# Kernel optimization log

Hardware: AMD Instinct MI355X
Metric: run time of the kernel (lower is better)

## Reference

```python
import jax, jax.numpy as jnp
import numpy as np
from jax import lax

EPS_RADIUS = 1e-3  # eps_radius from __init__


def setup_inputs() -> dict:
    key = jax.random.key(0)
    ks = jax.random.split(key, 8)
    Bsz, L, H, N, O = 16, 4096, 512, 512, 512
    n_pairs = N // 2
    return {
        "input": jax.random.normal(ks[0], (Bsz, L, H), dtype=jnp.float32),
        "state": jnp.zeros((Bsz, N), dtype=jnp.float32),
        "S": 0.1 * jax.random.normal(ks[1], (N, N), dtype=jnp.float32),
        "rho_raw": 0.01 * jax.random.normal(ks[2], (n_pairs,), dtype=jnp.float32),
        "theta": 0.01 * jax.random.normal(ks[3], (n_pairs,), dtype=jnp.float32),
        "K12_raw": 0.5 * jax.random.normal(ks[4], (N, H), dtype=jnp.float32),
        "K21_raw": 0.5 * jax.random.normal(ks[5], (O, N), dtype=jnp.float32),
        "K22_raw": 0.5 * jax.random.normal(ks[6], (O, H), dtype=jnp.float32),
        "log_gamma": jnp.zeros((), dtype=jnp.float32),  # gamma = 1.0
    }


def _dense_ssm_matrices(S, rho_raw, theta, K12_raw, K21_raw, K22_raw, log_gamma):
    N = S.shape[0]
    n_pairs = N // 2
    # K11 structured: block-diag 2x2 rotation-scaling blocks
    rho = jax.nn.sigmoid(rho_raw) * (1.0 - EPS_RADIUS)
    c, s = jnp.cos(theta), jnp.sin(theta)
    ii = jnp.arange(n_pairs) * 2
    K11 = jnp.zeros((N, N), dtype=S.dtype)
    K11 = (K11.at[ii, ii].set(rho * c)
               .at[ii, ii + 1].set(-rho * s)
               .at[ii + 1, ii].set(rho * s)
               .at[ii + 1, ii + 1].set(rho * c))
    # assemble full K and spectrally normalize (exact norm via SVD)
    K_raw = jnp.block([[K11, K12_raw], [K21_raw, K22_raw]])
    sigma = jnp.maximum(jnp.linalg.norm(K_raw, ord=2), 1e-5)
    K = K_raw / (sigma + 0.002)
    K11n = K[:N, :N]
    K12n = K[:N, N:]
    K21n = K[N:, :N]
    K22n = K[N:, N:]
    gamma = jnp.exp(log_gamma)
    Sinv = jnp.linalg.inv(S)
    A = Sinv @ K11n @ S          # (N, N)
    B = gamma * (Sinv @ K12n)    # (N, H)
    C = K21n @ S                 # (O, N)
    D = gamma * K22n             # (O, H)
    return A, B, C, D


def reference(input, state, S, rho_raw, theta, K12_raw, K21_raw, K22_raw, log_gamma):
    A, B, C, D = _dense_ssm_matrices(S, rho_raw, theta, K12_raw, K21_raw, K22_raw, log_gamma)
    u = input  # (Bsz, L, H)
    Bu = jnp.einsum('blh,nh->lbn', u, B)  # precompute input projections, (L, Bsz, N)

    def step(x, bu_t):
        x_new = x @ A.T + bu_t  # (Bsz, N)
        return x_new, x_new

    _, xs = lax.scan(step, state, Bu)  # xs: (L, Bsz, N), states x_1..x_L
    # y_t = C x_t + D u_t uses pre-states x_0..x_{L-1}
    pre = jnp.concatenate([state[None], xs[:-1]], axis=0)  # (L, Bsz, N)
    y = jnp.einsum('lbn,on->blo', pre, C) + jnp.einsum('blh,oh->blo', u, D)
    return y
```

## Files before the change

kernel.cpp:

```cpp
#include <hip/hip_runtime.h>
#include <stdint.h>


#define LM 40
#define CHUNK 128
#define WARM 12
#define LBLK 32

typedef float f32x4 __attribute__((ext_vector_type(4)));
typedef __bf16 bf16x8 __attribute__((ext_vector_type(8)));
typedef unsigned int u32;
typedef unsigned long long u64;
typedef unsigned short u16;

static __device__ __forceinline__ u16 f2bf(float f){
  u32 u = __float_as_uint(f);
  u32 r = (u + 0x7fffu + ((u >> 16) & 1u)) >> 16;
  return (u16)r;
}

static __device__ __forceinline__ float kraw_at(int i, int j,
    const float* rho_raw, const float* theta,
    const float* K12, const float* K21, const float* K22){
  if (i < 512){
    if (j < 512){
      if ((i >> 1) != (j >> 1)) return 0.f;
      int p = i >> 1;
      float rho = (1.f / (1.f + expf(-rho_raw[p]))) * 0.999f;
      float c = cosf(theta[p]), s = sinf(theta[p]);
      return ((i & 1) == 0) ? (((j & 1) == 0) ? rho * c : -rho * s)
                            : (((j & 1) == 0) ? rho * s :  rho * c);
    }
    return K12[i * 512 + (j - 512)];
  }
  if (j < 512) return K21[(i - 512) * 512 + j];
  return K22[(i - 512) * 512 + (j - 512)];
}

__global__ __launch_bounds__(256) void build_KT(const float* rho_raw, const float* theta,
    const float* K12, const float* K21, const float* K22, u16* KTbf,
    double* alpha, double* nrm2, u64* rec){
  if (blockIdx.x == 4096){
    int t = threadIdx.x;
    if (t < 64){ alpha[t] = 0.0; nrm2[t] = 0.0; }
    for (int i = t; i < 2048; i += 256) rec[i] = 0ull;
    return;
  }
  int idx = blockIdx.x * 256 + threadIdx.x;
  int j = idx >> 10, i = idx & 1023;
  KTbf[idx] = f2bf(kraw_at(i, j, rho_raw, theta, K12, K21, K22));
}

__global__ __launch_bounds__(256, 1) void lanczos_G(const float* __restrict__ G,
    u64* rec, double* alphaOut, double* nrm2Out){
  __shared__ __align__(16) float vl[1024];
  __shared__ float red[8];
  int t = threadIdx.x, wave = t >> 6, lane = t & 63;
  int row0 = blockIdx.x * 32;

  f32x4 greg[8][4];
  {
    const float* gbase = G + (size_t)(row0 + wave * 8) * 1024 + lane * 4;
    #pragma unroll
    for (int rr = 0; rr < 8; ++rr)
      #pragma unroll
      for (int i2 = 0; i2 < 4; ++i2)
        greg[rr][i2] = *(const f32x4*)(gbase + (size_t)rr * 1024 + i2 * 256);
  }

  float vprevreg[4] = {0.f, 0.f, 0.f, 0.f};
  float n2tot;
  {
    float s = 0.f;
    #pragma unroll
    for (int k = 0; k < 4; ++k){
      int i = t + 256 * k;
      float v = sinf(0.613f * (float)i + 0.271f) + 0.3f * sinf(0.0247f * (float)i + 1.3f);
      vl[i] = v;
      s += v * v;
    }
    #pragma unroll
    for (int off = 32; off; off >>= 1) s += __shfl_down(s, off);
    if (lane == 0) red[wave] = s;
    __syncthreads();
    n2tot = (red[0] + red[1]) + (red[2] + red[3]);
  }
  float scal = 1.f / sqrtf(n2tot);
  float betacoef = 0.f;

  for (int j = 1; j <= LM; ++j){
    u64* rb = rec + ((j & 1) ? 0 : 1024);
    {
      f32x4 vreg[4];
      #pragma unroll
      for (int i2 = 0; i2 < 4; ++i2)
        vreg[i2] = *((const f32x4*)vl + lane + 64 * i2);
      u64 myrec = 0ull;
      #pragma unroll
      for (int rr = 0; rr < 8; ++rr){
        float s = 0.f;
        #pragma unroll
        for (int i2 = 0; i2 < 4; ++i2){
          f32x4 g = greg[rr][i2], v = vreg[i2];
          s += g[0] * v[0] + g[1] * v[1] + g[2] * v[2] + g[3] * v[3];
        }
        #pragma unroll
        for (int off = 32; off; off >>= 1) s += __shfl_xor(s, off);
        if (lane == rr)
          myrec = ((u64)(u32)j << 32) | (u64)__float_as_uint(s);
      }
      if (lane < 8)
        __hip_atomic_store(&rb[row0 + wave * 8 + lane], myrec,
                           __ATOMIC_RELAXED, __HIP_MEMORY_SCOPE_AGENT);
    }

    float yr[4], vr[4];
    {
      u32 need = 0xFu;
      u64 rv[4];
      while (need){
        #pragma unroll
        for (int k = 0; k < 4; ++k){
          if (need & (1u << k)){
            u64 r = __hip_atomic_load(&rb[t + 256 * k],
                                      __ATOMIC_RELAXED, __HIP_MEMORY_SCOPE_AGENT);
            if ((u32)(r >> 32) == (u32)j){ rv[k] = r; need &= ~(1u << k); }
          }
        }
        if (need) __builtin_amdgcn_s_sleep(1);
      }
      #pragma unroll
      for (int k = 0; k < 4; ++k){
        yr[k] = __uint_as_float((u32)rv[k]);
        vr[k] = vl[t + 256 * k];
      }
    }

    float dotp = 0.f;
    #pragma unroll
    for (int k = 0; k < 4; ++k) dotp += vr[k] * yr[k];
    #pragma unroll
    for (int off = 32; off; off >>= 1) dotp += __shfl_down(dotp, off);
    if (lane == 0) red[wave] = dotp;
    __syncthreads();
    float dot = (red[0] + red[1]) + (red[2] + red[3]);
    float alpha_f = dot * scal * scal;

    float n2 = 0.f;
    #pragma unroll
    for (int k = 0; k < 4; ++k){
      float vh = vr[k] * scal;
      float wv = yr[k] * scal - alpha_f * vh - betacoef * vprevreg[k];
      vprevreg[k] = vh;
      vl[t + 256 * k] = wv;
      n2 += wv * wv;
    }
    #pragma unroll
    for (int off = 32; off; off >>= 1) n2 += __shfl_down(n2, off);
    if (lane == 0) red[4 + wave] = n2;
    __syncthreads();
    n2tot = (red[4] + red[5]) + (red[6] + red[7]);
    if (n2tot < 1e-30f) n2tot = 1e-30f;

    if (blockIdx.x == 0 && t == 0){
      alphaOut[j] = (double)alpha_f;
      nrm2Out[j]  = (double)n2tot;
    }
    betacoef = sqrtf(n2tot);
    scal = 1.f / betacoef;
  }
}

__global__ __launch_bounds__(256) void finalize_sigma(const double* alpha, const double* beta2,
    const float* rho_raw, const float* theta, const float* log_gamma,
    float* scal, float2* coef){
  __shared__ double sa[LM], sb2[LM + 1];
  __shared__ float sh_inv;
  int t = threadIdx.x;
  if (t < LM) sa[t] = alpha[t];
  if (t < LM + 1) sb2[t] = beta2[t];
  __syncthreads();
  if (t < 64){
    int lane = t;
    double lo = sa[0], hi = sa[0], bmax = 0.0;
    for (int i = 0; i < LM; ++i){
      if (sa[i] > lo) lo = sa[i];
      double bl = (i > 0) ? sqrt(fmax(sb2[i], 0.0)) : 0.0;
      double br = (i < LM - 1) ? sqrt(fmax(sb2[i + 1], 0.0)) : 0.0;
      double g = sa[i] + bl + br;
      if (g > hi) hi = g;
      if (i < LM - 1 && sb2[i + 1] > bmax) bmax = sb2[i + 1];
    }
    hi = hi + 1e-6 * fabs(hi) + 1e-20;
    lo = lo - 1e-6 * fabs(lo) - 1e-20;
    double pivmin = 1e-30 * bmax + 1e-300;
    for (int round = 0; round < 6; ++round){
      double x = lo + (hi - lo) * ((double)(lane + 1) / 65.0);
      double d = sa[0] - x; int cnt = (d < 0.0);
      for (int i = 1; i < LM; ++i){
        if (fabs(d) < pivmin) d = -pivmin;
        d = (sa[i] - x) - sb2[i] / d;
        cnt += (d < 0.0);
      }
      unsigned long long mk = __ballot(cnt >= LM);
      int bpos = (mk == 0ULL) ? 64 : (__ffsll((unsigned long long)mk) - 1);
      double xlo = __shfl(x, (bpos == 0) ? 0 : bpos - 1);
      double xhi = __shfl(x, (bpos == 64) ? 63 : bpos);
      double nlo = (bpos == 0) ? lo : xlo;
      double nhi = (bpos == 64) ? hi : xhi;
      lo = nlo; hi = nhi;
    }
    if (lane == 0){
      double lam = 0.5 * (lo + hi);
      double sig = (lam > 0.0) ? sqrt(lam) : 0.0;
      if (sig < 1e-5) sig = 1e-5;
      double spp = sig + 0.002;
      float inv = (float)(1.0 / spp);
      float g = expf(log_gamma[0]);
      scal[0] = inv; scal[1] = g; scal[2] = g * inv;
      sh_inv = inv;
    }
  }
  __syncthreads();
  float inv = sh_inv;
  float rho = (1.f / (1.f + expf(-rho_raw[t]))) * 0.999f;
  float c = cosf(theta[t]), s = sinf(theta[t]);
  coef[t] = make_float2(rho * c * inv, rho * s * inv);
}

__global__ __launch_bounds__(256) void prep_main(const float4* u4, u16* X,
    const float4* k12_4, u16* W12, const float* S, const float* state, float* w0){
  int blk = blockIdx.x;
  if (blk < 32768){
    long g = (long)blk * 256 + threadIdx.x;
    float4 v = u4[g];
    int h4 = (int)(g & 127);
    long row = g >> 7;
    u16* dst = X + row * 1024 + 512 + h4 * 4;
    u32 lo = (u32)f2bf(v.x) | ((u32)f2bf(v.y) << 16);
    u32 hi = (u32)f2bf(v.z) | ((u32)f2bf(v.w) << 16);
    *((uint2*)dst) = make_uint2(lo, hi);
  } else if (blk < 32768 + 256){
    long g = (long)(blk - 32768) * 256 + threadIdx.x;
    float4 v = k12_4[g];
    u32 lo = (u32)f2bf(v.x) | ((u32)f2bf(v.y) << 16);
    u32 hi = (u32)f2bf(v.z) | ((u32)f2bf(v.w) << 16);
    ((uint2*)W12)[g] = make_uint2(lo, hi);
  } else {
    int idx = (blk - 33024) * 256 + threadIdx.x;
    int b = idx >> 9, n = idx & 511;
    const float* sr = S + n * 512;
    const float* st = state + b * 512;
    float acc = 0.f;
    for (int m2 = 0; m2 < 512; ++m2) acc += sr[m2] * st[m2];
    w0[idx] = acc;
  }
}

__global__ __launch_bounds__(256) void build_wcat(const float* K21, const float* K22,
    const float* scal, u16* W){
  int idx = blockIdx.x * 256 + threadIdx.x;
  int o = idx >> 10, c = idx & 1023;
  float inv = scal[0], gi = scal[2];
  float v = (c < 512) ? K21[o * 512 + c] * inv : K22[o * 512 + (c - 512)] * gi;
  W[idx] = f2bf(v);
}

__global__ __launch_bounds__(256) void scan_kernel(const u32* Bu, const float2* coef,
    const float* w0, const float* scal, u16* X){
  int b = blockIdx.x >> 5;
  int c = blockIdx.x & 31;
  int p = threadIdx.x;
  float2 ab = coef[p];
  float gi = scal[2];
  int t0 = c * CHUNK;
  float wx, wy; int t;
  if (c == 0){ wx = w0[b * 512 + 2 * p]; wy = w0[b * 512 + 2 * p + 1]; t = 0; }
  else { wx = 0.f; wy = 0.f; t = t0 - WARM; }
  const u32* bub = Bu + (size_t)b * 4096 * 256;
  u16* xb = X + (size_t)b * 4096 * 1024;
  for (; t < t0; ++t){
    u32 v = bub[(size_t)t * 256 + p];
    float bx = __uint_as_float(v << 16);
    float by = __uint_as_float(v & 0xffff0000u);
    float nx = ab.x * wx - ab.y * wy + gi * bx;
    float ny = ab.y * wx + ab.x * wy + gi * by;
    wx = nx; wy = ny;
  }
  for (; t < t0 + CHUNK; ++t){
    u32 pk = (u32)f2bf(wx) | ((u32)f2bf(wy) << 16);
    *(u32*)(xb + (size_t)t * 1024 + 2 * p) = pk;
    u32 v = bub[(size_t)t * 256 + p];
    float bx = __uint_as_float(v << 16);
    float by = __uint_as_float(v & 0xffff0000u);
    float nx = ab.x * wx - ab.y * wy + gi * bx;
    float ny = ab.y * wx + ab.x * wy + gi * by;
    wx = nx; wy = ny;
  }
}

static __device__ __forceinline__ void gload16(const u16* g, u16* l){
  __builtin_amdgcn_global_load_lds((const __attribute__((address_space(1))) u32*)g,
                                   (__attribute__((address_space(3))) u32*)l, 16, 0, 0);
}

template <typename OT>
__global__ __launch_bounds__(256) void gemm_nt(const u16* __restrict__ A, int lda,
    const u16* __restrict__ B, int ldb, OT* __restrict__ C, int ldc, int K, int ntn){
  __shared__ u16 As[128 * 64];
  __shared__ u16 Bs[128 * 64];
  int g = blockIdx.x;
  int xcd = g & 7, local = g >> 3;
  int mper = gridDim.x >> 3; mper /= ntn;
  int bn = local % ntn;
  int bm = xcd * mper + local / ntn;
  int t = threadIdx.x, lane = t & 63, wave = t >> 6;
  int lrow = t >> 3;
  int swz = (((t & 7) ^ (lrow & 7)) << 3);
  const u16* Ag = A + (size_t)(bm * 128 + lrow) * lda + swz;
  const u16* Bg = B + (size_t)(bn * 128 + lrow) * ldb + swz;
  u16* Asd = As + t * 8;
  u16* Bsd = Bs + t * 8;
  f32x4 acc[4][4];
  #pragma unroll
  for (int mi = 0; mi < 4; ++mi)
    #pragma unroll
    for (int ni = 0; ni < 4; ++ni) acc[mi][ni] = (f32x4){0.f, 0.f, 0.f, 0.f};
  int wm = (wave & 1) << 6, wn = (wave >> 1) << 6;
  int fr = lane & 15, cbb = lane >> 4;
  for (int kt = 0; kt < K; kt += 64){
    __syncthreads();
    #pragma unroll
    for (int r = 0; r < 4; ++r){
      gload16(Ag + (size_t)(r * 32) * lda + kt, Asd + r * 2048);
      gload16(Bg + (size_t)(r * 32) * ldb + kt, Bsd + r * 2048);
    }
    __syncthreads();
    #pragma unroll
    for (int kk = 0; kk < 2; ++kk){
      bf16x8 af[4], bfr[4];
      #pragma unroll
      for (int mi = 0; mi < 4; ++mi){
        int row = wm + mi * 16 + fr;
        int pcb = ((kk << 2) + cbb) ^ (fr & 7);
        af[mi] = *(const bf16x8*)(As + row * 64 + pcb * 8);
      }
      #pragma unroll
      for (int ni = 0; ni < 4; ++ni){
        int row = wn + ni * 16 + fr;
        int pcb = ((kk << 2) + cbb) ^ (fr & 7);
        bfr[ni] = *(const bf16x8*)(Bs + row * 64 + pcb * 8);
      }
      #pragma unroll
      for (int mi = 0; mi < 4; ++mi)
        #pragma unroll
        for (int ni = 0; ni < 4; ++ni)
          acc[mi][ni] = __builtin_amdgcn_mfma_f32_16x16x32_bf16(af[mi], bfr[ni], acc[mi][ni], 0, 0, 0);
    }
  }
  int rq = lane >> 4;
  #pragma unroll
  for (int mi = 0; mi < 4; ++mi)
    #pragma unroll
    for (int ni = 0; ni < 4; ++ni){
      size_t base = (size_t)(bm * 128 + wm + mi * 16 + rq * 4) * ldc
                  + (size_t)(bn * 128 + wn + ni * 16 + fr);
      #pragma unroll
      for (int r = 0; r < 4; ++r){
        if constexpr (sizeof(OT) == 4) C[base + (size_t)r * ldc] = acc[mi][ni][r];
        else                           C[base + (size_t)r * ldc] = (OT)f2bf(acc[mi][ni][r]);
      }
    }
}

extern "C" void kernel_launch(void* const* d_in, const int* in_sizes, int n_in,
                              void* d_out, int out_size, void* d_ws, size_t ws_size,
                              hipStream_t stream){
  const float* u        = (const float*)d_in[0];
  const float* state    = (const float*)d_in[1];
  const float* S        = (const float*)d_in[2];
  const float* rho_raw  = (const float*)d_in[3];
  const float* theta    = (const float*)d_in[4];
  const float* K12      = (const float*)d_in[5];
  const float* K21      = (const float*)d_in[6];
  const float* K22      = (const float*)d_in[7];
  const float* log_gamma= (const float*)d_in[8];

  char* w = (char*)d_ws;
  size_t off = 0;
  auto alloc = [&](size_t bytes)->void*{
    void* p = w + off;
    off = (off + bytes + 255) & ~(size_t)255;
    return p;
  };
  double* alpha = (double*)alloc(64 * 8);
  double* nrm2  = (double*)alloc(64 * 8);
  u64*    rec   = (u64*)alloc(2048 * 8);
  float*  scal  = (float*)alloc(64);
  float2* coef  = (float2*)alloc(256 * 8);
  float*  w0    = (float*)alloc(16 * 512 * 4);
  u16*    KTbf  = (u16*)alloc((size_t)1024 * 1024 * 2);
  float*  G     = (float*)alloc((size_t)1024 * 1024 * 4);
  u16*    W12   = (u16*)alloc((size_t)512 * 512 * 2);
  u16*    Wcat  = (u16*)alloc((size_t)512 * 1024 * 2);
  u16*    Xb    = (u16*)alloc((size_t)65536 * 1024 * 2);
  u16*    Bu    = (u16*)d_out;

  build_KT<<<4097, 256, 0, stream>>>(rho_raw, theta, K12, K21, K22, KTbf, alpha, nrm2, rec);
  gemm_nt<float><<<64, 256, 0, stream>>>(KTbf, 1024, KTbf, 1024, G, 1024, 1024, 8);
  lanczos_G<<<LBLK, 256, 0, stream>>>(G, rec, alpha, nrm2);
  finalize_sigma<<<1, 256, 0, stream>>>(alpha + 1, nrm2, rho_raw, theta, log_gamma, scal, coef);

  prep_main<<<33056, 256, 0, stream>>>((const float4*)u, Xb, (const float4*)K12, W12, S, state, w0);
  build_wcat<<<2048, 256, 0, stream>>>(K21, K22, scal, Wcat);

  gemm_nt<u16><<<2048, 256, 0, stream>>>(Xb + 512, 1024, W12, 512, Bu, 512, 512, 4);
  scan_kernel<<<512, 256, 0, stream>>>((const u32*)Bu, coef, w0, scal, Xb);
  gemm_nt<float><<<2048, 256, 0, stream>>>(Xb, 1024, Wcat, 1024, (float*)d_out, 512, 1024, 4);
}
```

Measured before the change: 618.2 us.

## Merge pipeline stages into fewer launches, overlapping Lanczos with the input GEMM

Cuts the launch sequence from nine kernels to five. Independent work now shares a grid: the Gram GEMM runs alongside the input bf16 conversion, and the Lanczos spectral-norm blocks run alongside the Bu GEMM. The sigma finalization moves into Lanczos block 0, and the Wcat build moves into the scan kernel. This is meant to hide the latency-bound Lanczos iterations and the small kernels behind bulk work and to remove launch gaps. The risk is that the spin-waiting Lanczos blocks must all be co-resident with 2048 GEMM blocks, and the GEMM blocks now pay for the Lanczos kernel's shared memory.

```diff
diff --git a/kernel.cpp b/kernel.cpp
--- a/kernel.cpp
+++ b/kernel.cpp
@@ -37,24 +37,136 @@
   return K22[(i - 512) * 512 + (j - 512)];
 }
 
-__global__ __launch_bounds__(256) void build_KT(const float* rho_raw, const float* theta,
+static __device__ __forceinline__ void gload16(const u16* g, u16* l){
+  __builtin_amdgcn_global_load_lds((const __attribute__((address_space(1))) u32*)g,
+                                   (__attribute__((address_space(3))) u32*)l, 16, 0, 0);
+}
+
+template <typename OT>
+static __device__ __forceinline__ void gemm_body(int g, int ngrid,
+    const u16* __restrict__ A, int lda, const u16* __restrict__ B, int ldb,
+    OT* __restrict__ C, int ldc, int K, int ntn){
+  __shared__ u16 As[128 * 64];
+  __shared__ u16 Bs[128 * 64];
+  int xcd = g & 7, local = g >> 3;
+  int mper = (ngrid >> 3) / ntn;
+  int bn = local % ntn;
+  int bm = xcd * mper + local / ntn;
+  int t = threadIdx.x, lane = t & 63, wave = t >> 6;
+  int lrow = t >> 3;
+  int swz = (((t & 7) ^ (lrow & 7)) << 3);
+  const u16* Ag = A + (size_t)(bm * 128 + lrow) * lda + swz;
+  const u16* Bg = B + (size_t)(bn * 128 + lrow) * ldb + swz;
+  u16* Asd = As + t * 8;
+  u16* Bsd = Bs + t * 8;
+  f32x4 acc[4][4];
+  #pragma unroll
+  for (int mi = 0; mi < 4; ++mi)
+    #pragma unroll
+    for (int ni = 0; ni < 4; ++ni) acc[mi][ni] = (f32x4){0.f, 0.f, 0.f, 0.f};
+  int wm = (wave & 1) << 6, wn = (wave >> 1) << 6;
+  int fr = lane & 15, cbb = lane >> 4;
+  for (int kt = 0; kt < K; kt += 64){
+    __syncthreads();
+    #pragma unroll
+    for (int r = 0; r < 4; ++r){
+      gload16(Ag + (size_t)(r * 32) * lda + kt, Asd + r * 2048);
+      gload16(Bg + (size_t)(r * 32) * ldb + kt, Bsd + r * 2048);
+    }
+    __syncthreads();
+    #pragma unroll
+    for (int kk = 0; kk < 2; ++kk){
+      bf16x8 af[4], bfr[4];
+      #pragma unroll
+      for (int mi = 0; mi < 4; ++mi){
+        int row = wm + mi * 16 + fr;
+        int pcb = ((kk << 2) + cbb) ^ (fr & 7);
+        af[mi] = *(const bf16x8*)(As + row * 64 + pcb * 8);
+      }
+      #pragma unroll
+      for (int ni = 0; ni < 4; ++ni){
+        int row = wn + ni * 16 + fr;
+        int pcb = ((kk << 2) + cbb) ^ (fr & 7);
+        bfr[ni] = *(const bf16x8*)(Bs + row * 64 + pcb * 8);
+      }
+      #pragma unroll
+      for (int mi = 0; mi < 4; ++mi)
+        #pragma unroll
+        for (int ni = 0; ni < 4; ++ni)
+          acc[mi][ni] = __builtin_amdgcn_mfma_f32_16x16x32_bf16(af[mi], bfr[ni], acc[mi][ni], 0, 0, 0);
+    }
+  }
+  int rq = lane >> 4;
+  #pragma unroll
+  for (int mi = 0; mi < 4; ++mi)
+    #pragma unroll
+    for (int ni = 0; ni < 4; ++ni){
+      size_t base = (size_t)(bm * 128 + wm + mi * 16 + rq * 4) * ldc
+                  + (size_t)(bn * 128 + wn + ni * 16 + fr);
+      #pragma unroll
+      for (int r = 0; r < 4; ++r){
+        if constexpr (sizeof(OT) == 4) C[base + (size_t)r * ldc] = acc[mi][ni][r];
+        else                           C[base + (size_t)r * ldc] = (OT)f2bf(acc[mi][ni][r]);
+      }
+    }
+}
+
+__global__ __launch_bounds__(256) void kA(const float* rho_raw, const float* theta,
     const float* K12, const float* K21, const float* K22, u16* KTbf,
-    double* alpha, double* nrm2, u64* rec){
-  if (blockIdx.x == 4096){
-    int t = threadIdx.x;
-    if (t < 64){ alpha[t] = 0.0; nrm2[t] = 0.0; }
-    for (int i = t; i < 2048; i += 256) rec[i] = 0ull;
+    const float4* k12_4, u16* W12, u64* rec){
+  int blk = blockIdx.x;
+  if (blk < 4096){
+    int idx = blk * 256 + threadIdx.x;
+    int j = idx >> 10, i = idx & 1023;
+    KTbf[idx] = f2bf(kraw_at(i, j, rho_raw, theta, K12, K21, K22));
+  } else if (blk < 4096 + 256){
+    long g = (long)(blk - 4096) * 256 + threadIdx.x;
+    float4 v = k12_4[g];
+    u32 lo = (u32)f2bf(v.x) | ((u32)f2bf(v.y) << 16);
+    u32 hi = (u32)f2bf(v.z) | ((u32)f2bf(v.w) << 16);
+    ((uint2*)W12)[g] = make_uint2(lo, hi);
+  } else {
+    for (int i = threadIdx.x; i < 2048; i += 256) rec[i] = 0ull;
+  }
+}
+
+__global__ __launch_bounds__(256) void kB(const u16* KTbf, float* G,
+    const float4* u4, u16* X, const float* S, const float* state, float* w0){
+  int blk = blockIdx.x;
+  if (blk < 64){
+    gemm_body<float>(blk, 64, KTbf, 1024, KTbf, 1024, G, 1024, 1024, 8);
+  } else if (blk < 64 + 32768){
+    long g = (long)(blk - 64) * 256 + threadIdx.x;
+    float4 v = u4[g];
+    int h4 = (int)(g & 127);
+    long row = g >> 7;
+    u16* dst = X + row * 1024 + 512 + h4 * 4;
+    u32 lo = (u32)f2bf(v.x) | ((u32)f2bf(v.y) << 16);
+    u32 hi = (u32)f2bf(v.z) | ((u32)f2bf(v.w) << 16);
+    *((uint2*)dst) = make_uint2(lo, hi);
+  } else {
+    int idx = (blk - 32832) * 256 + threadIdx.x;
+    int b = idx >> 9, n = idx & 511;
+    const float* sr = S + n * 512;
+    const float* st = state + b * 512;
+    float acc = 0.f;
+    for (int m2 = 0; m2 < 512; ++m2) acc += sr[m2] * st[m2];
+    w0[idx] = acc;
+  }
+}
+
+__global__ __launch_bounds__(256, 1) void kC(const float* __restrict__ G,
+    u64* rec, const float* rho_raw, const float* theta, const float* log_gamma,
+    float* scal, float2* coef,
+    const u16* Xb, const u16* W12, u16* Bu){
+  if (blockIdx.x >= LBLK){
+    gemm_body<u16>(blockIdx.x - LBLK, 2048, Xb, 1024, W12, 512, Bu, 512, 512, 4);
     return;
   }
-  int idx = blockIdx.x * 256 + threadIdx.x;
-  int j = idx >> 10, i = idx & 1023;
-  KTbf[idx] = f2bf(kraw_at(i, j, rho_raw, theta, K12, K21, K22));
-}
-
-__global__ __launch_bounds__(256, 1) void lanczos_G(const float* __restrict__ G,
-    u64* rec, double* alphaOut, double* nrm2Out){
   __shared__ __align__(16) float vl[1024];
   __shared__ float red[8];
+  __shared__ double sa[LM], sb2[LM + 1];
+  __shared__ float sh_inv;
   int t = threadIdx.x, wave = t >> 6, lane = t & 63;
   int row0 = blockIdx.x * 32;
 
@@ -85,8 +197,9 @@
     __syncthreads();
     n2tot = (red[0] + red[1]) + (red[2] + red[3]);
   }
-  float scal = 1.f / sqrtf(n2tot);
+  float scl = 1.f / sqrtf(n2tot);
   float betacoef = 0.f;
+  if (t == 0) sb2[0] = 0.0;
 
   for (int j = 1; j <= LM; ++j){
     u64* rb = rec + ((j & 1) ? 0 : 1024);
@@ -116,24 +229,21 @@
 
     float yr[4], vr[4];
     {
-      u32 need = 0xFu;
-      u64 rv[4];
-      while (need){
-        #pragma unroll
-        for (int k = 0; k < 4; ++k){
-          if (need & (1u << k)){
-            u64 r = __hip_atomic_load(&rb[t + 256 * k],
-                                      __ATOMIC_RELAXED, __HIP_MEMORY_SCOPE_AGENT);
-            if ((u32)(r >> 32) == (u32)j){ rv[k] = r; need &= ~(1u << k); }
-          }
-        }
-        if (need) __builtin_amdgcn_s_sleep(1);
-      }
-      #pragma unroll
-      for (int k = 0; k < 4; ++k){
-        yr[k] = __uint_as_float((u32)rv[k]);
-        vr[k] = vl[t + 256 * k];
-      }
+      u64 r0, r1, r2, r3;
+      bool done = false;
+      while (!done){
+        r0 = __hip_atomic_load(&rb[t        ], __ATOMIC_RELAXED, __HIP_MEMORY_SCOPE_AGENT);
+        r1 = __hip_atomic_load(&rb[t +  256 ], __ATOMIC_RELAXED, __HIP_MEMORY_SCOPE_AGENT);
+        r2 = __hip_atomic_load(&rb[t +  512 ], __ATOMIC_RELAXED, __HIP_MEMORY_SCOPE_AGENT);
+        r3 = __hip_atomic_load(&rb[t +  768 ], __ATOMIC_RELAXED, __HIP_MEMORY_SCOPE_AGENT);
+        done = ((u32)(r0 >> 32) == (u32)j) && ((u32)(r1 >> 32) == (u32)j)
+            && ((u32)(r2 >> 32) == (u32)j) && ((u32)(r3 >> 32) == (u32)j);
+        if (!done) __builtin_amdgcn_s_sleep(1);
+      }
+      yr[0] = __uint_as_float((u32)r0); yr[1] = __uint_as_float((u32)r1);
+      yr[2] = __uint_as_float((u32)r2); yr[3] = __uint_as_float((u32)r3);
+      #pragma unroll
+      for (int k = 0; k < 4; ++k) vr[k] = vl[t + 256 * k];
     }
 
     float dotp = 0.f;
@@ -144,13 +254,13 @@
     if (lane == 0) red[wave] = dotp;
     __syncthreads();
     float dot = (red[0] + red[1]) + (red[2] + red[3]);
-    float alpha_f = dot * scal * scal;
+    float alpha_f = dot * scl * scl;
 
     float n2 = 0.f;
     #pragma unroll
     for (int k = 0; k < 4; ++k){
-      float vh = vr[k] * scal;
-      float wv = yr[k] * scal - alpha_f * vh - betacoef * vprevreg[k];
+      float vh = vr[k] * scl;
+      float wv = yr[k] * scl - alpha_f * vh - betacoef * vprevreg[k];
       vprevreg[k] = vh;
       vl[t + 256 * k] = wv;
       n2 += wv * wv;
@@ -162,26 +272,15 @@
     n2tot = (red[4] + red[5]) + (red[6] + red[7]);
     if (n2tot < 1e-30f) n2tot = 1e-30f;
 
-    if (blockIdx.x == 0 && t == 0){
-      alphaOut[j] = (double)alpha_f;
-      nrm2Out[j]  = (double)n2tot;
-    }
+    if (t == 0){ sa[j - 1] = (double)alpha_f; sb2[j] = (double)n2tot; }
     betacoef = sqrtf(n2tot);
-    scal = 1.f / betacoef;
-  }
-}
-
-__global__ __launch_bounds__(256) void finalize_sigma(const double* alpha, const double* beta2,
-    const float* rho_raw, const float* theta, const float* log_gamma,
-    float* scal, float2* coef){
-  __shared__ double sa[LM], sb2[LM + 1];
-  __shared__ float sh_inv;
-  int t = threadIdx.x;
-  if (t < LM) sa[t] = alpha[t];
-  if (t < LM + 1) sb2[t] = beta2[t];
+    scl = 1.f / betacoef;
+  }
+
+  if (blockIdx.x != 0) return;
   __syncthreads();
   if (t < 64){
-    int lane = t;
+    int lane2 = t;
     double lo = sa[0], hi = sa[0], bmax = 0.0;
     for (int i = 0; i < LM; ++i){
       if (sa[i] > lo) lo = sa[i];
@@ -195,7 +294,7 @@
     lo = lo - 1e-6 * fabs(lo) - 1e-20;
     double pivmin = 1e-30 * bmax + 1e-300;
     for (int round = 0; round < 6; ++round){
-      double x = lo + (hi - lo) * ((double)(lane + 1) / 65.0);
+      double x = lo + (hi - lo) * ((double)(lane2 + 1) / 65.0);
       double d = sa[0] - x; int cnt = (d < 0.0);
       for (int i = 1; i < LM; ++i){
         if (fabs(d) < pivmin) d = -pivmin;
@@ -210,7 +309,7 @@
       double nhi = (bpos == 64) ? hi : xhi;
       lo = nlo; hi = nhi;
     }
-    if (lane == 0){
+    if (lane2 == 0){
       double lam = 0.5 * (lo + hi);
       double sig = (lam > 0.0) ? sqrt(lam) : 0.0;
       if (sig < 1e-5) sig = 1e-5;
@@ -228,48 +327,20 @@
   coef[t] = make_float2(rho * c * inv, rho * s * inv);
 }
 
-__global__ __launch_bounds__(256) void prep_main(const float4* u4, u16* X,
-    const float4* k12_4, u16* W12, const float* S, const float* state, float* w0){
+__global__ __launch_bounds__(256) void kD(const u32* Bu, const float2* coef,
+    const float* w0, const float* scal, u16* X,
+    const float* K21, const float* K22, u16* W){
   int blk = blockIdx.x;
-  if (blk < 32768){
-    long g = (long)blk * 256 + threadIdx.x;
-    float4 v = u4[g];
-    int h4 = (int)(g & 127);
-    long row = g >> 7;
-    u16* dst = X + row * 1024 + 512 + h4 * 4;
-    u32 lo = (u32)f2bf(v.x) | ((u32)f2bf(v.y) << 16);
-    u32 hi = (u32)f2bf(v.z) | ((u32)f2bf(v.w) << 16);
-    *((uint2*)dst) = make_uint2(lo, hi);
-  } else if (blk < 32768 + 256){
-    long g = (long)(blk - 32768) * 256 + threadIdx.x;
-    float4 v = k12_4[g];
-    u32 lo = (u32)f2bf(v.x) | ((u32)f2bf(v.y) << 16);
-    u32 hi = (u32)f2bf(v.z) | ((u32)f2bf(v.w) << 16);
-    ((uint2*)W12)[g] = make_uint2(lo, hi);
-  } else {
-    int idx = (blk - 33024) * 256 + threadIdx.x;
-    int b = idx >> 9, n = idx & 511;
-    const float* sr = S + n * 512;
-    const float* st = state + b * 512;
-    float acc = 0.f;
-    for (int m2 = 0; m2 < 512; ++m2) acc += sr[m2] * st[m2];
-    w0[idx] = acc;
-  }
-}
-
-__global__ __launch_bounds__(256) void build_wcat(const float* K21, const float* K22,
-    const float* scal, u16* W){
-  int idx = blockIdx.x * 256 + threadIdx.x;
-  int o = idx >> 10, c = idx & 1023;
-  float inv = scal[0], gi = scal[2];
-  float v = (c < 512) ? K21[o * 512 + c] * inv : K22[o * 512 + (c - 512)] * gi;
-  W[idx] = f2bf(v);
-}
-
-__global__ __launch_bounds__(256) void scan_kernel(const u32* Bu, const float2* coef,
-    const float* w0, const float* scal, u16* X){
-  int b = blockIdx.x >> 5;
-  int c = blockIdx.x & 31;
+  if (blk >= 512){
+    int idx = (blk - 512) * 256 + threadIdx.x;
+    int o = idx >> 10, c = idx & 1023;
+    float inv = scal[0], gi = scal[2];
+    float v = (c < 512) ? K21[o * 512 + c] * inv : K22[o * 512 + (c - 512)] * gi;
+    W[idx] = f2bf(v);
+    return;
+  }
+  int b = blk >> 5;
+  int c = blk & 31;
   int p = threadIdx.x;
   float2 ab = coef[p];
   float gi = scal[2];
@@ -299,78 +370,10 @@
   }
 }
 
-static __device__ __forceinline__ void gload16(const u16* g, u16* l){
-  __builtin_amdgcn_global_load_lds((const __attribute__((address_space(1))) u32*)g,
-                                   (__attribute__((address_space(3))) u32*)l, 16, 0, 0);
-}
-
 template <typename OT>
 __global__ __launch_bounds__(256) void gemm_nt(const u16* __restrict__ A, int lda,
     const u16* __restrict__ B, int ldb, OT* __restrict__ C, int ldc, int K, int ntn){
-  __shared__ u16 As[128 * 64];
-  __shared__ u16 Bs[128 * 64];
-  int g = blockIdx.x;
-  int xcd = g & 7, local = g >> 3;
-  int mper = gridDim.x >> 3; mper /= ntn;
-  int bn = local % ntn;
-  int bm = xcd * mper + local / ntn;
-  int t = threadIdx.x, lane = t & 63, wave = t >> 6;
-  int lrow = t >> 3;
-  int swz = (((t & 7) ^ (lrow & 7)) << 3);
-  const u16* Ag = A + (size_t)(bm * 128 + lrow) * lda + swz;
-  const u16* Bg = B + (size_t)(bn * 128 + lrow) * ldb + swz;
-  u16* Asd = As + t * 8;
-  u16* Bsd = Bs + t * 8;
-  f32x4 acc[4][4];
-  #pragma unroll
-  for (int mi = 0; mi < 4; ++mi)
-    #pragma unroll
-    for (int ni = 0; ni < 4; ++ni) acc[mi][ni] = (f32x4){0.f, 0.f, 0.f, 0.f};
-  int wm = (wave & 1) << 6, wn = (wave >> 1) << 6;
-  int fr = lane & 15, cbb = lane >> 4;
-  for (int kt = 0; kt < K; kt += 64){
-    __syncthreads();
-    #pragma unroll
-    for (int r = 0; r < 4; ++r){
-      gload16(Ag + (size_t)(r * 32) * lda + kt, Asd + r * 2048);
-      gload16(Bg + (size_t)(r * 32) * ldb + kt, Bsd + r * 2048);
-    }
-    __syncthreads();
-    #pragma unroll
-    for (int kk = 0; kk < 2; ++kk){
-      bf16x8 af[4], bfr[4];
-      #pragma unroll
-      for (int mi = 0; mi < 4; ++mi){
-        int row = wm + mi * 16 + fr;
-        int pcb = ((kk << 2) + cbb) ^ (fr & 7);
-        af[mi] = *(const bf16x8*)(As + row * 64 + pcb * 8);
-      }
-      #pragma unroll
-      for (int ni = 0; ni < 4; ++ni){
-        int row = wn + ni * 16 + fr;
-        int pcb = ((kk << 2) + cbb) ^ (fr & 7);
-        bfr[ni] = *(const bf16x8*)(Bs + row * 64 + pcb * 8);
-      }
-      #pragma unroll
-      for (int mi = 0; mi < 4; ++mi)
-        #pragma unroll
-        for (int ni = 0; ni < 4; ++ni)
-          acc[mi][ni] = __builtin_amdgcn_mfma_f32_16x16x32_bf16(af[mi], bfr[ni], acc[mi][ni], 0, 0, 0);
-    }
-  }
-  int rq = lane >> 4;
-  #pragma unroll
-  for (int mi = 0; mi < 4; ++mi)
-    #pragma unroll
-    for (int ni = 0; ni < 4; ++ni){
-      size_t base = (size_t)(bm * 128 + wm + mi * 16 + rq * 4) * ldc
-                  + (size_t)(bn * 128 + wn + ni * 16 + fr);
-      #pragma unroll
-      for (int r = 0; r < 4; ++r){
-        if constexpr (sizeof(OT) == 4) C[base + (size_t)r * ldc] = acc[mi][ni][r];
-        else                           C[base + (size_t)r * ldc] = (OT)f2bf(acc[mi][ni][r]);
-      }
-    }
+  gemm_body<OT>(blockIdx.x, gridDim.x, A, lda, B, ldb, C, ldc, K, ntn);
 }
 
 extern "C" void kernel_launch(void* const* d_in, const int* in_sizes, int n_in,
@@ -393,8 +396,6 @@
     off = (off + bytes + 255) & ~(size_t)255;
     return p;
   };
-  double* alpha = (double*)alloc(64 * 8);
-  double* nrm2  = (double*)alloc(64 * 8);
   u64*    rec   = (u64*)alloc(2048 * 8);
   float*  scal  = (float*)alloc(64);
   float2* coef  = (float2*)alloc(256 * 8);
@@ -406,15 +407,11 @@
   u16*    Xb    = (u16*)alloc((size_t)65536 * 1024 * 2);
   u16*    Bu    = (u16*)d_out;
 
-  build_KT<<<4097, 256, 0, stream>>>(rho_raw, theta, K12, K21, K22, KTbf, alpha, nrm2, rec);
-  gemm_nt<float><<<64, 256, 0, stream>>>(KTbf, 1024, KTbf, 1024, G, 1024, 1024, 8);
-  lanczos_G<<<LBLK, 256, 0, stream>>>(G, rec, alpha, nrm2);
-  finalize_sigma<<<1, 256, 0, stream>>>(alpha + 1, nrm2, rho_raw, theta, log_gamma, scal, coef);
-
-  prep_main<<<33056, 256, 0, stream>>>((const float4*)u, Xb, (const float4*)K12, W12, S, state, w0);
-  build_wcat<<<2048, 256, 0, stream>>>(K21, K22, scal, Wcat);
-
-  gemm_nt<u16><<<2048, 256, 0, stream>>>(Xb + 512, 1024, W12, 512, Bu, 512, 512, 4);
-  scan_kernel<<<512, 256, 0, stream>>>((const u32*)Bu, coef, w0, scal, Xb);
+  kA<<<4353, 256, 0, stream>>>(rho_raw, theta, K12, K21, K22, KTbf,
+                               (const float4*)K12, W12, rec);
+  kB<<<32864, 256, 0, stream>>>(KTbf, G, (const float4*)u, Xb, S, state, w0);
+  kC<<<LBLK + 2048, 256, 0, stream>>>(G, rec, rho_raw, theta, log_gamma,
+                                      scal, coef, Xb + 512, W12, Bu);
+  kD<<<2560, 256, 0, stream>>>((const u32*)Bu, coef, w0, scal, Xb, K21, K22, Wcat);
   gemm_nt<float><<<2048, 256, 0, stream>>>(Xb, 1024, Wcat, 1024, (float*)d_out, 512, 1024, 4);
 }
```

Result: faster. 552.1 us (-10.7%).
